# Kernel optimization log

Hardware: AMD Instinct MI355X
Metric: run time of the kernel (lower is better)

The kernel has to match this reference:

```python
import jax, jax.numpy as jnp
import numpy as np

N_NODES = 50000
N_FEAT = 256
N_HID = 32
N_HEADS = 8
N_CLASSES = 32
N_EDGES = 800000
NEG_SLOPE = 0.2  # PyG GATConv default leaky_relu slope


def setup_inputs() -> dict:
    key = jax.random.key(0)
    ks = jax.random.split(key, 10)
    x = jax.random.normal(ks[0], (N_NODES, N_FEAT), dtype=jnp.float32)
    edge_index = jax.random.randint(ks[1], (2, N_EDGES), 0, N_NODES, dtype=jnp.int64)
    s1 = 1.0 / np.sqrt(N_FEAT)
    s2 = 1.0 / np.sqrt(N_HID * N_HEADS)
    W1 = jax.random.normal(ks[2], (N_FEAT, N_HEADS * N_HID), dtype=jnp.float32) * s1
    a_src1 = jax.random.normal(ks[3], (N_HEADS, N_HID), dtype=jnp.float32) * s1
    a_dst1 = jax.random.normal(ks[4], (N_HEADS, N_HID), dtype=jnp.float32) * s1
    b1 = jnp.zeros((N_HEADS * N_HID,), dtype=jnp.float32)
    W2 = jax.random.normal(ks[5], (N_HEADS * N_HID, N_CLASSES), dtype=jnp.float32) * s2
    a_src2 = jax.random.normal(ks[6], (1, N_CLASSES), dtype=jnp.float32) * s2
    a_dst2 = jax.random.normal(ks[7], (1, N_CLASSES), dtype=jnp.float32) * s2
    b2 = jnp.zeros((N_CLASSES,), dtype=jnp.float32)
    return {"x": x, "edge_index": edge_index, "W1": W1, "a_src1": a_src1,
            "a_dst1": a_dst1, "b1": b1, "W2": W2, "a_src2": a_src2,
            "a_dst2": a_dst2, "b2": b2}


def _gat_conv(h, src, dst, n_nodes, W, a_src, a_dst, heads, ch):
    # h: [N, F_in]; returns [N, heads, ch] aggregated per-node features
    z = (h @ W).reshape(n_nodes, heads, ch)           # [N,H,C]
    alpha_src = jnp.einsum('nhc,hc->nh', z, a_src)    # [N,H]
    alpha_dst = jnp.einsum('nhc,hc->nh', z, a_dst)    # [N,H]
    logits = jax.nn.leaky_relu(alpha_src[src] + alpha_dst[dst], NEG_SLOPE)  # [E,H]
    # segment softmax over incoming edges of each dst node
    m = jax.ops.segment_max(logits, dst, num_segments=n_nodes)  # [N,H]
    e = jnp.exp(logits - m[dst])                                 # [E,H]
    denom = jax.ops.segment_sum(e, dst, num_segments=n_nodes)   # [N,H]
    alpha = e / denom[dst]                                       # [E,H]
    msg = z[src] * alpha[:, :, None]                             # [E,H,C]
    return jax.ops.segment_sum(msg, dst, num_segments=n_nodes)  # [N,H,C]


def reference(x, edge_index, W1, a_src1, a_dst1, b1, W2, a_src2, a_dst2, b2):
    n = x.shape[0]
    # PyG GATConv default: add self loops
    loops = jnp.arange(n, dtype=edge_index.dtype)
    src = jnp.concatenate([edge_index[0], loops])
    dst = jnp.concatenate([edge_index[1], loops])
    h1 = _gat_conv(x, src, dst, n, W1, a_src1, a_dst1, N_HEADS, N_HID)
    h1 = h1.reshape(n, N_HEADS * N_HID) + b1          # concat=True
    h1 = jax.nn.elu(h1)
    # dropout is a no-op in eval mode
    h2 = _gat_conv(h1, src, dst, n, W2, a_src2, a_dst2, 1, N_CLASSES)
    out = h2.mean(axis=1) + b2                        # concat=False, heads=1
    return out
```

## Files before the change

kernel.cpp:

```cpp
#include <hip/hip_runtime.h>

#define NNODES 50000
#define NFEAT 256
#define NHID 32
#define NHEADS 8
#define NCLASSES 32
#define NEDGES 800000
#define ETOT (NEDGES + NNODES)
#define NSCAN_BLK 196
#define GEMM1_BLKS 782
#define SCAT_BLKS 3321
#define XCONV_BLKS 6250
#define AGG1_BLKS 25000

typedef __attribute__((ext_vector_type(8))) short short8;
typedef __attribute__((ext_vector_type(4))) float f32x4;

__device__ __forceinline__ void get_edge(const int* __restrict__ ei, int e,
                                         int& s, int& d) {
    if (e < NEDGES) { s = ei[e]; d = ei[NEDGES + e]; }
    else            { s = e - NEDGES; d = s; }
}
__device__ __forceinline__ float lrelu(float x) { return x > 0.f ? x : 0.2f * x; }
__device__ __forceinline__ unsigned short f2bf(float f) {
    unsigned u = __float_as_uint(f);
    unsigned r = u + 0x7fffu + ((u >> 16) & 1u);
    return (unsigned short)(r >> 16);
}
__device__ __forceinline__ float bflo(unsigned u) { return __uint_as_float(u << 16); }
__device__ __forceinline__ float bfhi(unsigned u) { return __uint_as_float(u & 0xffff0000u); }

__global__ void wprep_hist_k(const float* __restrict__ W1, const float* __restrict__ W2,
                             short8* __restrict__ W1frag, short8* __restrict__ W2frag,
                             const float* __restrict__ x, short8* __restrict__ xbf,
                             const int* __restrict__ ei, int* __restrict__ deg,
                             unsigned short* __restrict__ pos) {
    if (blockIdx.x < 36) {
        int idx = blockIdx.x * 256 + threadIdx.x;
        if (idx < 8192) {
            int kc = idx >> 10, r = idx & 1023;
            int nt = r >> 6, lane = r & 63;
            int l16 = lane & 15, quad = lane >> 4;
            int n = nt * 16 + l16, k0 = kc * 32 + quad * 8;
            short8 v;
#pragma unroll
            for (int j = 0; j < 8; ++j) v[j] = (short)f2bf(W1[(k0 + j) * 256 + n]);
            W1frag[idx] = v;
        } else if (idx < 8192 + 1024) {
            int g = idx - 8192;
            int kc = g >> 7, r = g & 127;
            int nt = r >> 6, lane = r & 63;
            int l16 = lane & 15, quad = lane >> 4;
            int n = nt * 16 + l16, k0 = kc * 32 + quad * 8;
            short8 v;
#pragma unroll
            for (int j = 0; j < 8; ++j) v[j] = (short)f2bf(W2[(k0 + j) * 32 + n]);
            W2frag[g] = v;
        }
    } else if (blockIdx.x < 36 + XCONV_BLKS) {
        int idx = (blockIdx.x - 36) * 256 + threadIdx.x;
        const float4* xp = (const float4*)(x + (size_t)idx * 8);
        float4 v0 = xp[0], v1 = xp[1];
        short8 o;
        o[0] = (short)f2bf(v0.x); o[1] = (short)f2bf(v0.y);
        o[2] = (short)f2bf(v0.z); o[3] = (short)f2bf(v0.w);
        o[4] = (short)f2bf(v1.x); o[5] = (short)f2bf(v1.y);
        o[6] = (short)f2bf(v1.z); o[7] = (short)f2bf(v1.w);
        xbf[idx] = o;
    } else {
        int e = (blockIdx.x - 36 - XCONV_BLKS) * 256 + threadIdx.x;
        if (e >= ETOT) return;
        int d = (e < NEDGES) ? ei[NEDGES + e] : (e - NEDGES);
        pos[e] = (unsigned short)atomicAdd(&deg[d], 1);
    }
}

__global__ void scan_part_k(const int* __restrict__ deg, int* __restrict__ row_local,
                            int* __restrict__ bsum) {
    __shared__ int ws[4];
    int t = threadIdx.x, lane = t & 63, wid = t >> 6;
    int idx = blockIdx.x * 256 + t;
    int v = (idx < NNODES) ? deg[idx] : 0;
    int inc = v;
#pragma unroll
    for (int off = 1; off < 64; off <<= 1) {
        int u = __shfl_up(inc, off, 64);
        if (lane >= off) inc += u;
    }
    if (lane == 63) ws[wid] = inc;
    __syncthreads();
    int woff = 0;
#pragma unroll
    for (int j = 0; j < 4; ++j) woff += (j < wid) ? ws[j] : 0;
    if (idx < NNODES) row_local[idx] = woff + inc - v;
    if (t == 255) bsum[blockIdx.x] = woff + inc;
}

__global__ void scan_fix_k(const int* __restrict__ row_local, const int* __restrict__ bsum,
                           int* __restrict__ row_start) {
    __shared__ int ws[4];
    __shared__ int sboff;
    int t = threadIdx.x, lane = t & 63, wid = t >> 6;
    int v = (t < NSCAN_BLK) ? bsum[t] : 0;
    int inc = v;
#pragma unroll
    for (int off = 1; off < 64; off <<= 1) {
        int u = __shfl_up(inc, off, 64);
        if (lane >= off) inc += u;
    }
    if (lane == 63) ws[wid] = inc;
    __syncthreads();
    int woff = 0;
#pragma unroll
    for (int j = 0; j < 4; ++j) woff += (j < wid) ? ws[j] : 0;
    if (t == blockIdx.x) sboff = woff + inc - v;
    __syncthreads();
    int idx = blockIdx.x * 256 + t;
    if (idx < NNODES) row_start[idx] = row_local[idx] + sboff;
    if (idx == 0) row_start[NNODES] = ETOT;
}

__global__ __launch_bounds__(256) void gemm1_scatter_k(
        const short8* __restrict__ xbf, const short8* __restrict__ Wfrag,
        const float* __restrict__ av, const float* __restrict__ bv,
        unsigned short* __restrict__ z1T, float* __restrict__ asT, float* __restrict__ adT,
        const int* __restrict__ ei, const int* __restrict__ row_start,
        const unsigned short* __restrict__ pos, int* __restrict__ csr_src) {
    if (blockIdx.x >= GEMM1_BLKS) {
        int e = (blockIdx.x - GEMM1_BLKS) * 256 + threadIdx.x;
        if (e >= ETOT) return;
        int s, d;
        get_edge(ei, e, s, d);
        csr_src[row_start[d] + (int)pos[e]] = s;
        return;
    }
    int t = threadIdx.x;
    int w = t >> 6, lane = t & 63;
    int quad = lane >> 4, l16 = lane & 15;
    int mA = blockIdx.x * 64 + w * 16 + l16;
    int mAl = min(mA, NNODES - 1);

    const short8* xr = xbf + (size_t)mAl * 32;
    short8 xreg[8];
#pragma unroll
    for (int kc = 0; kc < 8; ++kc) xreg[kc] = xr[kc * 4 + quad];

    f32x4 acc[16];
#pragma unroll
    for (int nt = 0; nt < 16; ++nt) acc[nt] = (f32x4){0.f, 0.f, 0.f, 0.f};

#pragma unroll
    for (int kc = 0; kc < 8; ++kc) {
        short8 af = xreg[kc];
#pragma unroll
        for (int nt = 0; nt < 16; ++nt) {
            short8 bf8 = Wfrag[kc * 1024 + nt * 64 + lane];
            acc[nt] = __builtin_amdgcn_mfma_f32_16x16x32_bf16(af, bf8, acc[nt], 0, 0, 0);
        }
    }
    int mrow0 = blockIdx.x * 64 + w * 16 + quad * 4;
#pragma unroll
    for (int nt = 0; nt < 16; ++nt) {
        int hh = nt >> 1, cc = (nt & 1) * 16 + l16;
#pragma unroll
        for (int r = 0; r < 4; ++r) {
            int mr = mrow0 + r;
            if (mr < NNODES)
                z1T[((size_t)hh * NNODES + mr) * 32 + cc] = f2bf(acc[nt][r]);
        }
    }
#pragma unroll
    for (int h = 0; h < 8; ++h) {
        float av0 = av[(2 * h) * 16 + l16], av1v = av[(2 * h + 1) * 16 + l16];
        float bv0 = bv[(2 * h) * 16 + l16], bv1v = bv[(2 * h + 1) * 16 + l16];
#pragma unroll
        for (int r = 0; r < 4; ++r) {
            float pa = acc[2 * h][r] * av0 + acc[2 * h + 1][r] * av1v;
            float pb = acc[2 * h][r] * bv0 + acc[2 * h + 1][r] * bv1v;
#pragma unroll
            for (int off = 1; off < 16; off <<= 1) {
                pa += __shfl_xor(pa, off, 64);
                pb += __shfl_xor(pb, off, 64);
            }
            int mr = mrow0 + r;
            if (l16 == 0 && mr < NNODES) {
                asT[(size_t)h * NNODES + mr] = pa;
                adT[(size_t)h * NNODES + mr] = pb;
            }
        }
    }
}

__global__ __launch_bounds__(256) void gemm2_mfma_k(
        const unsigned short* __restrict__ h1, const short8* __restrict__ Wfrag,
        const float* __restrict__ av, const float* __restrict__ bv,
        unsigned short* __restrict__ z2b, float* __restrict__ as_, float* __restrict__ ad_) {
    int w = threadIdx.x >> 6, lane = threadIdx.x & 63;
    int quad = lane >> 4, l16 = lane & 15;
    int mA = blockIdx.x * 64 + w * 16 + l16;
    int mAl = min(mA, NNODES - 1);

    f32x4 acc[2];
    acc[0] = (f32x4){0.f, 0.f, 0.f, 0.f};
    acc[1] = (f32x4){0.f, 0.f, 0.f, 0.f};
    for (int kc = 0; kc < 8; ++kc) {
        int k0 = kc * 32 + quad * 8;
        short8 af = *(const short8*)(h1 + (size_t)mAl * 256 + k0);
#pragma unroll
        for (int nt = 0; nt < 2; ++nt) {
            short8 bf8 = Wfrag[kc * 128 + nt * 64 + lane];
            acc[nt] = __builtin_amdgcn_mfma_f32_16x16x32_bf16(af, bf8, acc[nt], 0, 0, 0);
        }
    }
    int mrow0 = blockIdx.x * 64 + w * 16 + quad * 4;
    float av0 = av[l16], av1v = av[16 + l16];
    float bv0 = bv[l16], bv1v = bv[16 + l16];
#pragma unroll
    for (int r = 0; r < 4; ++r) {
        int mr = mrow0 + r;
        float pa = acc[0][r] * av0 + acc[1][r] * av1v;
        float pb = acc[0][r] * bv0 + acc[1][r] * bv1v;
#pragma unroll
        for (int off = 1; off < 16; off <<= 1) {
            pa += __shfl_xor(pa, off, 64);
            pb += __shfl_xor(pb, off, 64);
        }
        if (mr < NNODES) {
            z2b[(size_t)mr * 32 + l16] = f2bf(acc[0][r]);
            z2b[(size_t)mr * 32 + 16 + l16] = f2bf(acc[1][r]);
            if (l16 == 0) { as_[mr] = pa; ad_[mr] = pb; }
        }
    }
}

__global__ __launch_bounds__(256) void agg1_csr_k(
        const int* __restrict__ row_start, const int* __restrict__ csr_src,
        const unsigned short* __restrict__ z1T, const float* __restrict__ asT,
        const float* __restrict__ adT, const float* __restrict__ b,
        unsigned short* __restrict__ h1) {
    int h = blockIdx.x & 7;
    int dblk = blockIdx.x >> 3;
    int g = dblk * 16 + (threadIdx.x >> 4);
    int l = threadIdx.x & 15;
    int lane = threadIdx.x & 63;
    int c0 = l * 2;
    const float* ash = asT + (size_t)h * NNODES;
    const unsigned short* zh = z1T + (size_t)h * NNODES * 32;
    int beg = row_start[g], end = row_start[g + 1];
    float adn = adT[(size_t)h * NNODES + g];
    int e8 = l & 7;
    int gb = lane & 48;
    float sum = 0.f, a0 = 0.f, a1 = 0.f;
    int i = beg;
    for (; i + 8 <= end; i += 8) {
        int sv = csr_src[i + e8];
        float myw = __expf(lrelu(ash[sv] + adn));
        int se[8];
        float we[8];
#pragma unroll
        for (int e = 0; e < 8; ++e) {
            se[e] = __shfl(sv, gb | e, 64);
            we[e] = __shfl(myw, gb | (8 | e), 64);
        }
        unsigned q[8];
#pragma unroll
        for (int e = 0; e < 8; ++e)
            q[e] = *(const unsigned*)(zh + (size_t)se[e] * 32 + c0);
#pragma unroll
        for (int e = 0; e < 8; ++e) {
            float wgt = we[e];
            sum += wgt;
            a0 += wgt * bflo(q[e]);
            a1 += wgt * bfhi(q[e]);
        }
    }
    for (; i < end; ++i) {
        int s = csr_src[i];
        float wgt = __expf(lrelu(ash[s] + adn));
        unsigned q = *(const unsigned*)(zh + (size_t)s * 32 + c0);
        sum += wgt;
        a0 += wgt * bflo(q);
        a1 += wgt * bfhi(q);
    }
    float inv = 1.f / sum;
    int cg = h * 32 + c0;
    float o0 = a0 * inv + b[cg];
    float o1 = a1 * inv + b[cg + 1];
    o0 = o0 > 0.f ? o0 : expm1f(o0);
    o1 = o1 > 0.f ? o1 : expm1f(o1);
    unsigned pk = (unsigned)f2bf(o0) | ((unsigned)f2bf(o1) << 16);
    *(unsigned*)(h1 + (size_t)g * 256 + cg) = pk;
}

__global__ void agg2_csr_k(const int* __restrict__ row_start, const int* __restrict__ csr_src,
                           const unsigned short* __restrict__ z2b, const float* __restrict__ as_,
                           const float* __restrict__ ad_, const float* __restrict__ b,
                           float* __restrict__ out) {
    int g = blockIdx.x * 16 + (threadIdx.x >> 4);
    int l = threadIdx.x & 15;
    int lane = threadIdx.x & 63;
    int c0 = l * 2;
    int beg = row_start[g], end = row_start[g + 1];
    float adn = ad_[g];
    int e8 = l & 7;
    int gb = lane & 48;
    float sum = 0.f, a0 = 0.f, a1 = 0.f;
    int i = beg;
    for (; i + 8 <= end; i += 8) {
        int sv = csr_src[i + e8];
        float myw = __expf(lrelu(as_[sv] + adn));
        int se[8];
        float we[8];
#pragma unroll
        for (int e = 0; e < 8; ++e) {
            se[e] = __shfl(sv, gb | e, 64);
            we[e] = __shfl(myw, gb | (8 | e), 64);
        }
        unsigned q[8];
#pragma unroll
        for (int e = 0; e < 8; ++e)
            q[e] = *(const unsigned*)(z2b + (size_t)se[e] * 32 + c0);
#pragma unroll
        for (int e = 0; e < 8; ++e) {
            float wgt = we[e];
            sum += wgt;
            a0 += wgt * bflo(q[e]);
            a1 += wgt * bfhi(q[e]);
        }
    }
    for (; i < end; ++i) {
        int s = csr_src[i];
        float wgt = __expf(lrelu(as_[s] + adn));
        unsigned q = *(const unsigned*)(z2b + (size_t)s * 32 + c0);
        sum += wgt;
        a0 += wgt * bflo(q);
        a1 += wgt * bfhi(q);
    }
    float inv = 1.f / sum;
    float2 o;
    o.x = a0 * inv + b[c0];
    o.y = a1 * inv + b[c0 + 1];
    *(float2*)(out + (size_t)g * 32 + c0) = o;
}

extern "C" void kernel_launch(void* const* d_in, const int* in_sizes, int n_in,
                              void* d_out, int out_size, void* d_ws, size_t ws_size,
                              hipStream_t stream) {
    const float* x   = (const float*)d_in[0];
    const int*   ei  = (const int*)d_in[1];
    const float* W1  = (const float*)d_in[2];
    const float* av1 = (const float*)d_in[3];
    const float* bv1 = (const float*)d_in[4];
    const float* b1  = (const float*)d_in[5];
    const float* W2  = (const float*)d_in[6];
    const float* av2 = (const float*)d_in[7];
    const float* bv2 = (const float*)d_in[8];
    const float* b2  = (const float*)d_in[9];
    float* out = (float*)d_out;

    unsigned short* z1T = (unsigned short*)d_ws;
    unsigned short* h1 = (unsigned short*)((float*)d_ws + 6400000);
    float* as1 = (float*)d_ws + 12800000;
    float* ad1 = as1 + 400000;
    unsigned short* z2b = (unsigned short*)(ad1 + 400000);
    float* as2 = ad1 + 400000 + 800000;
    float* ad2 = as2 + 50000;
    short8* W1frag = (short8*)(ad2 + 50000);
    short8* W2frag = W1frag + 8192;
    int* deg       = (int*)(ad2 + 50000) + 36864;
    int* row_start = deg + 50000;
    int* csr_src   = row_start + 50001;
    int* row_local = csr_src + 850000;
    int* bsum      = row_local + 50000;
    unsigned short* pos = (unsigned short*)z2b;
    short8* xbf = (short8*)h1;

    hipMemsetAsync(deg, 0, (size_t)50000 * 4, stream);

    wprep_hist_k<<<36 + XCONV_BLKS + SCAT_BLKS, 256, 0, stream>>>(
        W1, W2, W1frag, W2frag, x, xbf, ei, deg, pos);
    scan_part_k<<<NSCAN_BLK, 256, 0, stream>>>(deg, row_local, bsum);
    scan_fix_k<<<NSCAN_BLK, 256, 0, stream>>>(row_local, bsum, row_start);

    gemm1_scatter_k<<<GEMM1_BLKS + SCAT_BLKS, 256, 0, stream>>>(
        xbf, W1frag, av1, bv1, z1T, as1, ad1, ei, row_start, pos, csr_src);
    agg1_csr_k<<<AGG1_BLKS, 256, 0, stream>>>(row_start, csr_src, z1T, as1, ad1, b1, h1);

    gemm2_mfma_k<<<(NNODES + 63) / 64, 256, 0, stream>>>(h1, W2frag, av2, bv2, z2b, as2, ad2);
    agg2_csr_k<<<NNODES / 16, 256, 0, stream>>>(row_start, csr_src, z2b, as2, ad2, b2, out);
}
```

Baseline: 335.0 us.

## Use 8 lanes per node with 8-byte gathers and software-prefetched edge weights

Both aggregation kernels now assign 8 threads per destination node instead of 16, so each wave covers 8 nodes rather than 4 and each thread gathers 4 bf16 channels with a uint2 load. The next chunk of source indices and exp weights is loaded before the current chunk is processed, and the scalar tail loop is replaced by masked lanes with zero weight. This halves the thread count and the shuffle overhead per node and overlaps the index and logit loads with the feature gathers. In exchange each thread holds more accumulator registers, the padded tail wastes some lanes on low-degree nodes, and the out-of-range nodes in the last block need clamping.

After: 307.8 us. 8.1% less time.

```diff
diff --git a/kernel.cpp b/kernel.cpp
--- a/kernel.cpp
+++ b/kernel.cpp
@@ -11,7 +11,8 @@
 #define GEMM1_BLKS 782
 #define SCAT_BLKS 3321
 #define XCONV_BLKS 6250
-#define AGG1_BLKS 25000
+#define NDBLK 1563
+#define AGG1_BLKS (NDBLK * 8)
 
 typedef __attribute__((ext_vector_type(8))) short short8;
 typedef __attribute__((ext_vector_type(4))) float f32x4;
@@ -240,107 +241,123 @@
         unsigned short* __restrict__ h1) {
     int h = blockIdx.x & 7;
     int dblk = blockIdx.x >> 3;
-    int g = dblk * 16 + (threadIdx.x >> 4);
-    int l = threadIdx.x & 15;
     int lane = threadIdx.x & 63;
-    int c0 = l * 2;
+    int grp = threadIdx.x >> 3;
+    int c8 = threadIdx.x & 7;
+    int gb = lane & 56;
+    int g = dblk * 32 + grp;
+    int gl = min(g, NNODES - 1);
     const float* ash = asT + (size_t)h * NNODES;
     const unsigned short* zh = z1T + (size_t)h * NNODES * 32;
-    int beg = row_start[g], end = row_start[g + 1];
-    float adn = adT[(size_t)h * NNODES + g];
-    int e8 = l & 7;
-    int gb = lane & 48;
-    float sum = 0.f, a0 = 0.f, a1 = 0.f;
-    int i = beg;
-    for (; i + 8 <= end; i += 8) {
-        int sv = csr_src[i + e8];
-        float myw = __expf(lrelu(ash[sv] + adn));
+    int beg = row_start[gl], end = row_start[gl + 1];
+    float adn = adT[(size_t)h * NNODES + gl];
+    float sum = 0.f, a0 = 0.f, a1 = 0.f, a2 = 0.f, a3 = 0.f;
+
+    int idx = beg + c8;
+    int sv = csr_src[idx < end ? idx : end - 1];
+    float wmy = __expf(lrelu(ash[sv] + adn));
+    wmy = (idx < end) ? wmy : 0.f;
+
+    for (int i = beg; i < end; i += 8) {
+        int idx2 = i + 8 + c8;
+        int sv2 = csr_src[idx2 < end ? idx2 : end - 1];
+        float wmy2 = __expf(lrelu(ash[sv2] + adn));
+        wmy2 = (idx2 < end) ? wmy2 : 0.f;
+
         int se[8];
         float we[8];
 #pragma unroll
         for (int e = 0; e < 8; ++e) {
             se[e] = __shfl(sv, gb | e, 64);
-            we[e] = __shfl(myw, gb | (8 | e), 64);
-        }
-        unsigned q[8];
-#pragma unroll
-        for (int e = 0; e < 8; ++e)
-            q[e] = *(const unsigned*)(zh + (size_t)se[e] * 32 + c0);
+            we[e] = __shfl(wmy, gb | e, 64);
+        }
 #pragma unroll
         for (int e = 0; e < 8; ++e) {
-            float wgt = we[e];
-            sum += wgt;
-            a0 += wgt * bflo(q[e]);
-            a1 += wgt * bfhi(q[e]);
-        }
-    }
-    for (; i < end; ++i) {
-        int s = csr_src[i];
-        float wgt = __expf(lrelu(ash[s] + adn));
-        unsigned q = *(const unsigned*)(zh + (size_t)s * 32 + c0);
-        sum += wgt;
-        a0 += wgt * bflo(q);
-        a1 += wgt * bfhi(q);
-    }
-    float inv = 1.f / sum;
-    int cg = h * 32 + c0;
-    float o0 = a0 * inv + b[cg];
-    float o1 = a1 * inv + b[cg + 1];
-    o0 = o0 > 0.f ? o0 : expm1f(o0);
-    o1 = o1 > 0.f ? o1 : expm1f(o1);
-    unsigned pk = (unsigned)f2bf(o0) | ((unsigned)f2bf(o1) << 16);
-    *(unsigned*)(h1 + (size_t)g * 256 + cg) = pk;
-}
-
-__global__ void agg2_csr_k(const int* __restrict__ row_start, const int* __restrict__ csr_src,
-                           const unsigned short* __restrict__ z2b, const float* __restrict__ as_,
-                           const float* __restrict__ ad_, const float* __restrict__ b,
-                           float* __restrict__ out) {
-    int g = blockIdx.x * 16 + (threadIdx.x >> 4);
-    int l = threadIdx.x & 15;
+            uint2 q = *(const uint2*)(zh + (size_t)se[e] * 32 + c8 * 4);
+            float wg = we[e];
+            sum += wg;
+            a0 += wg * bflo(q.x);
+            a1 += wg * bfhi(q.x);
+            a2 += wg * bflo(q.y);
+            a3 += wg * bfhi(q.y);
+        }
+        sv = sv2;
+        wmy = wmy2;
+    }
+    if (g < NNODES) {
+        int cg = h * 32 + c8 * 4;
+        float inv = 1.f / sum;
+        float o0 = a0 * inv + b[cg + 0];
+        float o1 = a1 * inv + b[cg + 1];
+        float o2 = a2 * inv + b[cg + 2];
+        float o3 = a3 * inv + b[cg + 3];
+        o0 = o0 > 0.f ? o0 : expm1f(o0);
+        o1 = o1 > 0.f ? o1 : expm1f(o1);
+        o2 = o2 > 0.f ? o2 : expm1f(o2);
+        o3 = o3 > 0.f ? o3 : expm1f(o3);
+        uint2 pk;
+        pk.x = (unsigned)f2bf(o0) | ((unsigned)f2bf(o1) << 16);
+        pk.y = (unsigned)f2bf(o2) | ((unsigned)f2bf(o3) << 16);
+        *(uint2*)(h1 + (size_t)g * 256 + cg) = pk;
+    }
+}
+
+__global__ __launch_bounds__(256) void agg2_csr_k(
+        const int* __restrict__ row_start, const int* __restrict__ csr_src,
+        const unsigned short* __restrict__ z2b, const float* __restrict__ as_,
+        const float* __restrict__ ad_, const float* __restrict__ b,
+        float* __restrict__ out) {
     int lane = threadIdx.x & 63;
-    int c0 = l * 2;
-    int beg = row_start[g], end = row_start[g + 1];
-    float adn = ad_[g];
-    int e8 = l & 7;
-    int gb = lane & 48;
-    float sum = 0.f, a0 = 0.f, a1 = 0.f;
-    int i = beg;
-    for (; i + 8 <= end; i += 8) {
-        int sv = csr_src[i + e8];
-        float myw = __expf(lrelu(as_[sv] + adn));
+    int grp = threadIdx.x >> 3;
+    int c8 = threadIdx.x & 7;
+    int gb = lane & 56;
+    int g = blockIdx.x * 32 + grp;
+    int gl = min(g, NNODES - 1);
+    int beg = row_start[gl], end = row_start[gl + 1];
+    float adn = ad_[gl];
+    float sum = 0.f, a0 = 0.f, a1 = 0.f, a2 = 0.f, a3 = 0.f;
+
+    int idx = beg + c8;
+    int sv = csr_src[idx < end ? idx : end - 1];
+    float wmy = __expf(lrelu(as_[sv] + adn));
+    wmy = (idx < end) ? wmy : 0.f;
+
+    for (int i = beg; i < end; i += 8) {
+        int idx2 = i + 8 + c8;
+        int sv2 = csr_src[idx2 < end ? idx2 : end - 1];
+        float wmy2 = __expf(lrelu(as_[sv2] + adn));
+        wmy2 = (idx2 < end) ? wmy2 : 0.f;
+
         int se[8];
         float we[8];
 #pragma unroll
         for (int e = 0; e < 8; ++e) {
             se[e] = __shfl(sv, gb | e, 64);
-            we[e] = __shfl(myw, gb | (8 | e), 64);
-        }
-        unsigned q[8];
-#pragma unroll
-        for (int e = 0; e < 8; ++e)
-            q[e] = *(const unsigned*)(z2b + (size_t)se[e] * 32 + c0);
+            we[e] = __shfl(wmy, gb | e, 64);
+        }
 #pragma unroll
         for (int e = 0; e < 8; ++e) {
-            float wgt = we[e];
-            sum += wgt;
-            a0 += wgt * bflo(q[e]);
-            a1 += wgt * bfhi(q[e]);
-        }
-    }
-    for (; i < end; ++i) {
-        int s = csr_src[i];
-        float wgt = __expf(lrelu(as_[s] + adn));
-        unsigned q = *(const unsigned*)(z2b + (size_t)s * 32 + c0);
-        sum += wgt;
-        a0 += wgt * bflo(q);
-        a1 += wgt * bfhi(q);
-    }
-    float inv = 1.f / sum;
-    float2 o;
-    o.x = a0 * inv + b[c0];
-    o.y = a1 * inv + b[c0 + 1];
-    *(float2*)(out + (size_t)g * 32 + c0) = o;
+            uint2 q = *(const uint2*)(z2b + (size_t)se[e] * 32 + c8 * 4);
+            float wg = we[e];
+            sum += wg;
+            a0 += wg * bflo(q.x);
+            a1 += wg * bfhi(q.x);
+            a2 += wg * bflo(q.y);
+            a3 += wg * bfhi(q.y);
+        }
+        sv = sv2;
+        wmy = wmy2;
+    }
+    if (g < NNODES) {
+        int cg = c8 * 4;
+        float inv = 1.f / sum;
+        float4 o;
+        o.x = a0 * inv + b[cg + 0];
+        o.y = a1 * inv + b[cg + 1];
+        o.z = a2 * inv + b[cg + 2];
+        o.w = a3 * inv + b[cg + 3];
+        *(float4*)(out + (size_t)g * 32 + cg) = o;
+    }
 }
 
 extern "C" void kernel_launch(void* const* d_in, const int* in_sizes, int n_in,
@@ -387,5 +404,5 @@
     agg1_csr_k<<<AGG1_BLKS, 256, 0, stream>>>(row_start, csr_src, z1T, as1, ad1, b1, h1);
 
     gemm2_mfma_k<<<(NNODES + 63) / 64, 256, 0, stream>>>(h1, W2frag, av2, bv2, z2b, as2, ad2);
-    agg2_csr_k<<<NNODES / 16, 256, 0, stream>>>(row_start, csr_src, z2b, as2, ad2, b2, out);
-}
+    agg2_csr_k<<<NDBLK, 256, 0, stream>>>(row_start, csr_src, z2b, as2, ad2, b2, out);
+}
```
